# Kernel optimization log

Hardware: AMD Instinct MI355X
Metric: run time of the kernel (lower is better)

## Reference

```python
import jax, jax.numpy as jnp
import numpy as np

S, P, SAMPLE_K = 512, 512, 10          # superpoints, points per superpoint, FPS samples
NUM_MASKS, H, W = 128, 512, 512
RADIUS, MASK_THRES, SIM_THRES, N_MASK, TOP_K = 0.2, 0.2, 0.5, 5, 10
FEAT_DIM = 32


def setup_inputs() -> dict:
    key = jax.random.key(0)
    k1, k2, k3, k4, k5, k6 = jax.random.split(key, 6)
    N = S * P
    pcds = jax.random.normal(k1, (N, 3), jnp.float32) * 2.0
    spt_labels = (jnp.arange(N) // P).astype(jnp.int32)  # sorted, contiguous superpoints
    masks = jax.random.bernoulli(k2, 0.15, (NUM_MASKS, H, W))
    yx = jax.random.randint(k3, (N, 2), 0, H).astype(jnp.int32)
    vis = jax.random.randint(k4, (N, 1), 0, 2).astype(jnp.int32)
    mapping = jnp.concatenate([jnp.zeros((N, 1), jnp.int32), yx, vis], axis=1)
    sam_scores = jax.random.uniform(k5, (NUM_MASKS,), jnp.float32)
    point_feas = jax.random.normal(k6, (N, FEAT_DIM), jnp.float32)
    return {"pcds": pcds, "spt_labels": spt_labels, "masks": masks,
            "mapping": mapping, "sam_scores": sam_scores, "point_feas": point_feas}


def _fps(pts, k):
    # pts: (P,3). Deterministic first index 0 (torch uses a random first index).
    d0 = jnp.linalg.norm(pts - pts[0], axis=1)
    def step(dist, _):
        idx = jnp.argmax(dist)
        dist = jnp.minimum(dist, jnp.linalg.norm(pts - pts[idx], axis=1))
        return dist, idx
    _, idxs = jax.lax.scan(step, d0, None, length=k - 1)
    return jnp.concatenate([jnp.zeros((1,), idxs.dtype), idxs])


def reference(pcds, spt_labels, masks, mapping, sam_scores, point_feas):
    # ---- FPS representatives per superpoint (all superpoints have P>=min_points) ----
    pts_g = pcds.reshape(S, P, 3)
    idxs = jax.vmap(lambda p: _fps(p, SAMPLE_K))(pts_g)              # (S, k)
    reps = jnp.take_along_axis(pts_g, idxs[:, :, None], axis=1)      # (S, k, 3)

    # ---- pairwise min distance between superpoint rep sets -> radius adjacency ----
    flat = reps.reshape(S * SAMPLE_K, 3)
    sq = jnp.sum(flat * flat, axis=1)
    D2 = sq[:, None] + sq[None, :] - 2.0 * (flat @ flat.T)           # (S*k, S*k)
    D2 = D2.reshape(S, SAMPLE_K, S, SAMPLE_K).min(axis=(1, 3))       # (S, S)
    dmin = jnp.sqrt(jnp.maximum(D2, 1e-12))
    eye = jnp.eye(S, dtype=bool)
    adjacency = jnp.where((dmin < RADIUS) & (~eye), jnp.exp(-dmin), 0.0)

    # ---- per-point mask coverage (visible points only) ----
    y = jnp.clip(mapping[:, 1], 0, H - 1)
    x = jnp.clip(mapping[:, 2], 0, W - 1)
    vis = mapping[:, 3] == 1
    coverage = masks[:, y, x].T & vis[:, None]                       # (N, num_masks)

    # ---- aggregate coverage per superpoint, keep top_k superpoints per mask ----
    counts = coverage.reshape(S, P, NUM_MASKS).sum(axis=1)
    fraction = counts.astype(jnp.float32) / (P + 1e-6)               # (S, num_masks)
    _, top_inds = jax.lax.top_k(fraction.T, TOP_K)                   # (num_masks, top_k)
    topk_mask = jnp.zeros((NUM_MASKS, S), bool).at[
        jnp.arange(NUM_MASKS)[:, None], top_inds].set(True).T        # (S, num_masks)
    frac_kept = jnp.where(topk_mask, fraction, 0.0)
    contrib = frac_kept >= MASK_THRES                                # (S, num_masks) bool

    # ---- superpoint features (mean, L2-normalized) ----
    feats = point_feas.reshape(S, P, -1).sum(axis=1) / (P + 1e-6)
    feats = feats / jnp.maximum(jnp.linalg.norm(feats, axis=1, keepdims=True), 1e-12)

    # ---- modulate adjacency by top-n_mask mask-overlap IoU and feature similarity ----
    union = contrib[:, None, :] | contrib[None, :, :]                # (S, S, num_masks)
    _, u_inds = jax.lax.top_k(union.astype(jnp.float32), N_MASK)     # (S, S, n_mask)
    mi = jnp.take_along_axis(jnp.broadcast_to(contrib[:, None, :], union.shape), u_inds, axis=2)
    mj = jnp.take_along_axis(jnp.broadcast_to(contrib[None, :, :], union.shape), u_inds, axis=2)
    inter = (mi & mj).sum(-1).astype(jnp.float32)
    uni = (mi | mj).sum(-1).astype(jnp.float32)
    overlap = inter / (uni + 1e-6)
    sim = jnp.clip((feats @ feats.T + 1.0) / 2.0, 0.0, 1.0)
    sim = jnp.where(sim < SIM_THRES, 1.0, sim)
    mod = overlap * sim
    adjacency = jnp.where(adjacency > 0, jnp.maximum(mod, adjacency), adjacency)

    # ---- superpoint confidence scores ----
    weights = frac_kept * sam_scores[None, :]
    conf = jnp.maximum(weights.sum(1) / (frac_kept.sum(1) + 1e-6), 0.0)
    return adjacency, conf
```

## Files before the change

### kernel.cpp

```cpp
#include <hip/hip_runtime.h>
#include <cstddef>
#include <cstdint>

#define SPTS 512
#define PPS  512
#define KFPS 10
#define NMSK 128
#define HH 512
#define WW 512
#define HWPIX (HH*WW)
#define FDIM 32
#define TOPK_SEL 10
#define NMASK_TOP 5

__device__ __forceinline__ unsigned mask_val(const void* raw, long long idx, int mode) {
    if (mode == 0) return ((const unsigned char*)raw)[idx] ? 1u : 0u;
    if (mode == 1) return ((const int*)raw)[idx] ? 1u : 0u;
    return (((const float*)raw)[idx] != 0.0f) ? 1u : 0u;
}

__device__ __forceinline__ int detect_mode(const void* raw) {
    __shared__ int s_any1, s_any23;
    if (threadIdx.x == 0) { s_any1 = 0; s_any23 = 0; }
    __syncthreads();
    if (threadIdx.x < 256) {
        uint4 w = ((const uint4*)raw)[threadIdx.x];
        unsigned b1  = (w.x >> 8 | w.y >> 8 | w.z >> 8 | w.w >> 8) & 0xFFu;
        unsigned b23 = ((w.x >> 16) | (w.y >> 16) | (w.z >> 16) | (w.w >> 16)) & 0xFFFFu;
        if (b1)  atomicOr(&s_any1, 1);
        if (b23) atomicOr(&s_any23, 1);
    }
    __syncthreads();
    return s_any1 ? 0 : (s_any23 ? 2 : 1);
}

__global__ void __launch_bounds__(256) k_repack_fps(const void* raw, unsigned* maskbits,
                                                    const float* pcds, float* reps) {
    int bid = blockIdx.x;
    if (bid < 1024) {
        int mode = detect_mode(raw);
        int quarter = bid & 3;
        int ptile   = bid >> 2;
        int pix0 = ptile * 1024 + threadIdx.x * 4;
        unsigned w[4] = {0, 0, 0, 0};
        if (mode == 0) {
            const unsigned char* base = (const unsigned char*)raw + (size_t)quarter * 32 * HWPIX + pix0;
#pragma unroll
            for (int m = 0; m < 32; ++m) {
                unsigned v = *(const unsigned*)(base + (size_t)m * HWPIX);
#pragma unroll
                for (int p = 0; p < 4; ++p)
                    w[p] |= ((v >> (8 * p)) & 1u) << m;
            }
        } else {
            const unsigned* base = (const unsigned*)raw + (size_t)quarter * 32 * HWPIX + pix0;
#pragma unroll
            for (int m = 0; m < 32; ++m) {
                uint4 v = *(const uint4*)(base + (size_t)m * HWPIX);
                w[0] |= (unsigned)(v.x != 0u) << m;
                w[1] |= (unsigned)(v.y != 0u) << m;
                w[2] |= (unsigned)(v.z != 0u) << m;
                w[3] |= (unsigned)(v.w != 0u) << m;
            }
        }
#pragma unroll
        for (int p = 0; p < 4; ++p)
            maskbits[(size_t)(pix0 + p) * 4 + quarter] = w[p];
        return;
    }
    int lane = threadIdx.x & 63;
    int wv   = threadIdx.x >> 6;
    int s    = (bid - 1024) * 4 + wv;
    const float* base = pcds + (size_t)s * PPS * 3;
    float px_[8], py_[8], pz_[8];
#pragma unroll
    for (int k = 0; k < 8; ++k) {
        int p = lane + 64 * k;
        px_[k] = base[p * 3 + 0];
        py_[k] = base[p * 3 + 1];
        pz_[k] = base[p * 3 + 2];
    }
    float ax = __shfl(px_[0], 0), ay = __shfl(py_[0], 0), az = __shfl(pz_[0], 0);
    float dist[8];
#pragma unroll
    for (int k = 0; k < 8; ++k) {
        float dx = px_[k] - ax, dy = py_[k] - ay, dz = pz_[k] - az;
        dist[k] = sqrtf(dx * dx + dy * dy + dz * dz);
    }
    if (lane == 0) {
        reps[((size_t)s * KFPS + 0) * 3 + 0] = ax;
        reps[((size_t)s * KFPS + 0) * 3 + 1] = ay;
        reps[((size_t)s * KFPS + 0) * 3 + 2] = az;
    }
    for (int kk = 1; kk < KFPS; ++kk) {
        float bv = dist[0]; int bk = 0;
#pragma unroll
        for (int k = 1; k < 8; ++k)
            if (dist[k] > bv) { bv = dist[k]; bk = k; }
        float v = bv; int pidx = lane + 64 * bk;
#pragma unroll
        for (int off = 1; off < 64; off <<= 1) {
            float ov = __shfl_xor(v, off);
            int   op = __shfl_xor(pidx, off);
            if (ov > v || (ov == v && op < pidx)) { v = ov; pidx = op; }
        }
        int owner = pidx & 63, slot = pidx >> 6;
        float sx = px_[0], sy = py_[0], sz = pz_[0];
#pragma unroll
        for (int j = 1; j < 8; ++j)
            if (slot == j) { sx = px_[j]; sy = py_[j]; sz = pz_[j]; }
        sx = __shfl(sx, owner); sy = __shfl(sy, owner); sz = __shfl(sz, owner);
        if (lane == 0) {
            reps[((size_t)s * KFPS + kk) * 3 + 0] = sx;
            reps[((size_t)s * KFPS + kk) * 3 + 1] = sy;
            reps[((size_t)s * KFPS + kk) * 3 + 2] = sz;
        }
#pragma unroll
        for (int k = 0; k < 8; ++k) {
            float dx = px_[k] - sx, dy = py_[k] - sy, dz = pz_[k] - sz;
            float d = sqrtf(dx * dx + dy * dy + dz * dz);
            dist[k] = fminf(dist[k], d);
        }
    }
}

__global__ void __launch_bounds__(PPS) k_counts_feats(const int* mapping, const unsigned* maskbits,
                                                      const void* raw, int packed,
                                                      const float* feas,
                                                      int* counts, unsigned* contrib, float* feats) {
    int s = blockIdx.x;
    int t = threadIdx.x;
    if (t < 4) contrib[s * 4 + t] = 0u;
    __shared__ int cnt[NMSK];
    __shared__ float fpart[16][FDIM];
    if (t < NMSK) cnt[t] = 0;
    int mode = 0;
    if (!packed) mode = detect_mode(raw);
    __syncthreads();
    int i = s * PPS + t;
    int4 mp = ((const int4*)mapping)[i];
    int y = min(max(mp.y, 0), HH - 1);
    int x = min(max(mp.z, 0), WW - 1);
    bool vis = (mp.w == 1);
    unsigned w0 = 0, w1 = 0, w2 = 0, w3 = 0;
    if (vis) {
        if (packed) {
            uint4 v = *((const uint4*)(maskbits + (size_t)(y * WW + x) * 4));
            w0 = v.x; w1 = v.y; w2 = v.z; w3 = v.w;
        } else {
            long long pix = (long long)y * WW + x;
            for (int m = 0; m < NMSK; ++m) {
                unsigned v = mask_val(raw, (long long)m * HWPIX + pix, mode);
                if (m < 32)       w0 |= v << m;
                else if (m < 64)  w1 |= v << (m - 32);
                else if (m < 96)  w2 |= v << (m - 64);
                else              w3 |= v << (m - 96);
            }
        }
    }
    int lane = t & 63;
    unsigned ww[4] = { w0, w1, w2, w3 };
#pragma unroll
    for (int m = 0; m < NMSK; ++m) {
        unsigned bit = (ww[m >> 5] >> (m & 31)) & 1u;
        unsigned long long bal = __ballot((int)bit);
        if (lane == 0) atomicAdd(&cnt[m], (int)__popcll(bal));
    }
    {
        int g = t >> 5, d = t & 31;
        const float* fb = feas + (size_t)s * PPS * FDIM;
        float acc = 0.0f;
#pragma unroll 8
        for (int it = 0; it < 32; ++it) acc += fb[(g + 16 * it) * FDIM + d];
        fpart[g][d] = acc;
    }
    __syncthreads();
    if (t < NMSK) counts[s * NMSK + t] = cnt[t];
    if (t < FDIM) {
        float sum = 0.0f;
#pragma unroll
        for (int q = 0; q < 16; ++q) sum += fpart[q][t];
        float f = sum / 512.0f;
        float sq = f * f;
#pragma unroll
        for (int off = 16; off >= 1; off >>= 1) sq += __shfl_xor(sq, off);
        feats[s * FDIM + t] = f / fmaxf(sqrtf(sq), 1e-12f);
    }
}

__global__ void __launch_bounds__(SPTS) k_topk(const int* counts, unsigned* contrib, float* frac_kept) {
    int m = blockIdx.x;
    int s = threadIdx.x;
    __shared__ int cl[SPTS];
    cl[s] = counts[s * NMSK + m];
    __syncthreads();
    int c = cl[s];
    int rank = 0;
    for (int s2 = 0; s2 < SPTS; ++s2) {
        int c2 = cl[s2];
        rank += (c2 > c || (c2 == c && s2 < s)) ? 1 : 0;
    }
    bool sel = (rank < TOPK_SEL);
    float frac = (float)c / 512.0f;
    frac_kept[s * NMSK + m] = sel ? frac : 0.0f;
    if (sel && frac >= 0.2f)
        atomicOr(&contrib[s * 4 + (m >> 5)], 1u << (m & 31));
}

__global__ void __launch_bounds__(256) k_adjmod(const float* reps, const unsigned* contrib,
                                                const float* feats, const float* frac_kept,
                                                const float* sam, float* out) {
    if (blockIdx.x >= (SPTS * SPTS) / 256) {
        int s = (blockIdx.x - (SPTS * SPTS) / 256) * 256 + threadIdx.x;
        if (s < SPTS) {
            float sw = 0.0f, sf = 0.0f;
            for (int m = 0; m < NMSK; ++m) {
                float fk = frac_kept[s * NMSK + m];
                sw += fk * sam[m];
                sf += fk;
            }
            out[(size_t)SPTS * SPTS + s] = fmaxf(sw / (sf + 1e-6f), 0.0f);
        }
        return;
    }
    int idx = blockIdx.x * blockDim.x + threadIdx.x;
    int i = idx >> 9, j = idx & 511;
    __shared__ float ri[KFPS * 3];
    __shared__ float sqi[KFPS];
    if (threadIdx.x < KFPS * 3) ri[threadIdx.x] = reps[(size_t)i * KFPS * 3 + threadIdx.x];
    __syncthreads();
    if (threadIdx.x < KFPS) {
        float X = ri[threadIdx.x * 3], Y = ri[threadIdx.x * 3 + 1], Z = ri[threadIdx.x * 3 + 2];
        sqi[threadIdx.x] = X * X + Y * Y + Z * Z;
    }
    __syncthreads();
    float rjx[KFPS], rjy[KFPS], rjz[KFPS], sqj[KFPS];
    const float* rp = reps + (size_t)j * KFPS * 3;
#pragma unroll
    for (int b = 0; b < KFPS; ++b) {
        float X = rp[b * 3], Y = rp[b * 3 + 1], Z = rp[b * 3 + 2];
        rjx[b] = X; rjy[b] = Y; rjz[b] = Z;
        sqj[b] = X * X + Y * Y + Z * Z;
    }
    float mn = 1e30f;
#pragma unroll
    for (int a = 0; a < KFPS; ++a) {
        float ax = ri[a * 3], ay = ri[a * 3 + 1], az = ri[a * 3 + 2];
        float sa = sqi[a];
#pragma unroll
        for (int b = 0; b < KFPS; ++b) {
            float dot = ax * rjx[b] + ay * rjy[b] + az * rjz[b];
            float d2 = (sa + sqj[b]) - 2.0f * dot;
            mn = fminf(mn, d2);
        }
    }
    float dmin = sqrtf(fmaxf(mn, 1e-12f));
    float a = (dmin < 0.2f && i != j) ? expf(-dmin) : 0.0f;
    if (a > 0.0f) {
        uint4 c4i = *((const uint4*)(contrib + (size_t)i * 4));
        uint4 c4j = *((const uint4*)(contrib + (size_t)j * 4));
        unsigned cia[4] = { c4i.x, c4i.y, c4i.z, c4i.w };
        unsigned cja[4] = { c4j.x, c4j.y, c4j.z, c4j.w };
        int taken = 0, inter = 0, uni = 0;
#pragma unroll
        for (int w = 0; w < 4; ++w) {
            unsigned u = cia[w] | cja[w];
            unsigned both = cia[w] & cja[w];
            while (u && taken < NMASK_TOP) {
                unsigned bit = u & (~u + 1u);
                uni++;
                if (both & bit) inter++;
                u ^= bit; taken++;
            }
        }
        float overlap = (float)inter / ((float)uni + 1e-6f);
        const float* fi = feats + (size_t)i * FDIM;
        const float* fj = feats + (size_t)j * FDIM;
        float dot = 0.0f;
#pragma unroll
        for (int d = 0; d < FDIM; ++d) dot += fi[d] * fj[d];
        float sim = (dot + 1.0f) / 2.0f;
        sim = fminf(fmaxf(sim, 0.0f), 1.0f);
        if (sim < 0.5f) sim = 1.0f;
        a = fmaxf(overlap * sim, a);
    }
    out[idx] = a;
}

extern "C" void kernel_launch(void* const* d_in, const int* in_sizes, int n_in,
                              void* d_out, int out_size, void* d_ws, size_t ws_size,
                              hipStream_t stream) {
    const float* pcds    = (const float*)d_in[0];
    const void*  masks   = d_in[2];
    const int*   mapping = (const int*)d_in[3];
    const float* sam     = (const float*)d_in[4];
    const float* feas    = (const float*)d_in[5];
    float* out = (float*)d_out;

    char* ws = (char*)d_ws;
    size_t off = 0;
    auto take = [&](size_t bytes) -> void* {
        void* p = ws + off;
        off += (bytes + 255) & ~(size_t)255;
        return p;
    };
    float*    reps      = (float*)take((size_t)SPTS * KFPS * 3 * sizeof(float));
    int*      counts    = (int*)take((size_t)SPTS * NMSK * sizeof(int));
    unsigned* contrib   = (unsigned*)take((size_t)SPTS * 4 * sizeof(unsigned));
    float*    frac_kept = (float*)take((size_t)SPTS * NMSK * sizeof(float));
    float*    feats     = (float*)take((size_t)SPTS * FDIM * sizeof(float));
    unsigned* maskbits  = (unsigned*)take((size_t)HWPIX * 4 * sizeof(unsigned));
    size_t need_packed = off;
    int packed = (ws_size >= need_packed) ? 1 : 0;

    k_repack_fps<<<1152, 256, 0, stream>>>(masks, maskbits, pcds, reps);
    k_counts_feats<<<SPTS, PPS, 0, stream>>>(mapping, maskbits, masks, packed, feas,
                                             counts, contrib, feats);
    k_topk<<<NMSK, SPTS, 0, stream>>>(counts, contrib, frac_kept);
    k_adjmod<<<(SPTS * SPTS) / 256 + 2, 256, 0, stream>>>(reps, contrib, feats, frac_kept, sam, out);
}
```

Before: 80.50 us.

## Rebalance stages: move adjacency distance into stage2, feature means into stage1

Moves the per-superpoint feature averaging (now float4-vectorised) into the first kernel alongside mask repacking and FPS. Moves the pairwise rep-distance adjacency computation into the counts kernel so it overlaps with the bit counting, writing the base adjacency to the output. The last kernel then only reads that output and modulates the nonzero entries. Mask repacking now handles all 128 masks per thread and writes one uint4 per pixel instead of scattered 32-bit words. The cost is an extra full read of the output matrix and higher register pressure in the repack loop.

```diff
diff --git a/kernel.cpp b/kernel.cpp
--- a/kernel.cpp
+++ b/kernel.cpp
@@ -34,43 +34,7 @@
     return s_any1 ? 0 : (s_any23 ? 2 : 1);
 }
 
-__global__ void __launch_bounds__(256) k_repack_fps(const void* raw, unsigned* maskbits,
-                                                    const float* pcds, float* reps) {
-    int bid = blockIdx.x;
-    if (bid < 1024) {
-        int mode = detect_mode(raw);
-        int quarter = bid & 3;
-        int ptile   = bid >> 2;
-        int pix0 = ptile * 1024 + threadIdx.x * 4;
-        unsigned w[4] = {0, 0, 0, 0};
-        if (mode == 0) {
-            const unsigned char* base = (const unsigned char*)raw + (size_t)quarter * 32 * HWPIX + pix0;
-#pragma unroll
-            for (int m = 0; m < 32; ++m) {
-                unsigned v = *(const unsigned*)(base + (size_t)m * HWPIX);
-#pragma unroll
-                for (int p = 0; p < 4; ++p)
-                    w[p] |= ((v >> (8 * p)) & 1u) << m;
-            }
-        } else {
-            const unsigned* base = (const unsigned*)raw + (size_t)quarter * 32 * HWPIX + pix0;
-#pragma unroll
-            for (int m = 0; m < 32; ++m) {
-                uint4 v = *(const uint4*)(base + (size_t)m * HWPIX);
-                w[0] |= (unsigned)(v.x != 0u) << m;
-                w[1] |= (unsigned)(v.y != 0u) << m;
-                w[2] |= (unsigned)(v.z != 0u) << m;
-                w[3] |= (unsigned)(v.w != 0u) << m;
-            }
-        }
-#pragma unroll
-        for (int p = 0; p < 4; ++p)
-            maskbits[(size_t)(pix0 + p) * 4 + quarter] = w[p];
-        return;
-    }
-    int lane = threadIdx.x & 63;
-    int wv   = threadIdx.x >> 6;
-    int s    = (bid - 1024) * 4 + wv;
+__device__ __forceinline__ void fps_wave(const float* pcds, float* reps, int s, int lane) {
     const float* base = pcds + (size_t)s * PPS * 3;
     float px_[8], py_[8], pz_[8];
 #pragma unroll
@@ -124,67 +88,158 @@
     }
 }
 
-__global__ void __launch_bounds__(PPS) k_counts_feats(const int* mapping, const unsigned* maskbits,
-                                                      const void* raw, int packed,
-                                                      const float* feas,
-                                                      int* counts, unsigned* contrib, float* feats) {
-    int s = blockIdx.x;
+__global__ void __launch_bounds__(256) k_stage1(const void* raw, unsigned* maskbits,
+                                                const float* pcds, float* reps,
+                                                const float* feas, float* feats, int packed) {
+    int bid = blockIdx.x;
     int t = threadIdx.x;
-    if (t < 4) contrib[s * 4 + t] = 0u;
-    __shared__ int cnt[NMSK];
-    __shared__ float fpart[16][FDIM];
-    if (t < NMSK) cnt[t] = 0;
-    int mode = 0;
-    if (!packed) mode = detect_mode(raw);
-    __syncthreads();
-    int i = s * PPS + t;
-    int4 mp = ((const int4*)mapping)[i];
-    int y = min(max(mp.y, 0), HH - 1);
-    int x = min(max(mp.z, 0), WW - 1);
-    bool vis = (mp.w == 1);
-    unsigned w0 = 0, w1 = 0, w2 = 0, w3 = 0;
-    if (vis) {
-        if (packed) {
-            uint4 v = *((const uint4*)(maskbits + (size_t)(y * WW + x) * 4));
-            w0 = v.x; w1 = v.y; w2 = v.z; w3 = v.w;
+    if (bid < 256) {
+        if (!packed) return;
+        int mode = detect_mode(raw);
+        int pix0 = bid * 1024 + t * 4;
+        unsigned w[4][4] = {};
+        if (mode == 0) {
+            const unsigned char* base = (const unsigned char*)raw + pix0;
+#pragma unroll 8
+            for (int m = 0; m < NMSK; ++m) {
+                unsigned v = *(const unsigned*)(base + (size_t)m * HWPIX);
+                int q = m >> 5; unsigned sh = m & 31;
+#pragma unroll
+                for (int p = 0; p < 4; ++p)
+                    w[q][p] |= ((v >> (8 * p)) & 1u) << sh;
+            }
         } else {
-            long long pix = (long long)y * WW + x;
+            const unsigned* base = (const unsigned*)raw + pix0;
+#pragma unroll 8
             for (int m = 0; m < NMSK; ++m) {
-                unsigned v = mask_val(raw, (long long)m * HWPIX + pix, mode);
-                if (m < 32)       w0 |= v << m;
-                else if (m < 64)  w1 |= v << (m - 32);
-                else if (m < 96)  w2 |= v << (m - 64);
-                else              w3 |= v << (m - 96);
-            }
-        }
-    }
-    int lane = t & 63;
-    unsigned ww[4] = { w0, w1, w2, w3 };
-#pragma unroll
-    for (int m = 0; m < NMSK; ++m) {
-        unsigned bit = (ww[m >> 5] >> (m & 31)) & 1u;
-        unsigned long long bal = __ballot((int)bit);
-        if (lane == 0) atomicAdd(&cnt[m], (int)__popcll(bal));
+                uint4 v = *(const uint4*)(base + (size_t)m * HWPIX);
+                int q = m >> 5; unsigned sh = m & 31;
+                w[q][0] |= (unsigned)(v.x != 0u) << sh;
+                w[q][1] |= (unsigned)(v.y != 0u) << sh;
+                w[q][2] |= (unsigned)(v.z != 0u) << sh;
+                w[q][3] |= (unsigned)(v.w != 0u) << sh;
+            }
+        }
+#pragma unroll
+        for (int p = 0; p < 4; ++p) {
+            uint4 o; o.x = w[0][p]; o.y = w[1][p]; o.z = w[2][p]; o.w = w[3][p];
+            *(uint4*)(maskbits + (size_t)(pix0 + p) * 4) = o;
+        }
+        return;
+    }
+    if (bid < 384) {
+        fps_wave(pcds, reps, (bid - 256) * 4 + (t >> 6), t & 63);
+        return;
     }
     {
-        int g = t >> 5, d = t & 31;
+        int s = bid - 384;
         const float* fb = feas + (size_t)s * PPS * FDIM;
-        float acc = 0.0f;
-#pragma unroll 8
-        for (int it = 0; it < 32; ++it) acc += fb[(g + 16 * it) * FDIM + d];
-        fpart[g][d] = acc;
-    }
-    __syncthreads();
-    if (t < NMSK) counts[s * NMSK + t] = cnt[t];
-    if (t < FDIM) {
-        float sum = 0.0f;
-#pragma unroll
-        for (int q = 0; q < 16; ++q) sum += fpart[q][t];
-        float f = sum / 512.0f;
-        float sq = f * f;
-#pragma unroll
-        for (int off = 16; off >= 1; off >>= 1) sq += __shfl_xor(sq, off);
-        feats[s * FDIM + t] = f / fmaxf(sqrtf(sq), 1e-12f);
+        int c = t & 7, g = t >> 3;
+        float4 acc = { 0.0f, 0.0f, 0.0f, 0.0f };
+#pragma unroll 4
+        for (int it = 0; it < 16; ++it) {
+            int p = g + 32 * it;
+            float4 v = *(const float4*)(fb + p * FDIM + c * 4);
+            acc.x += v.x; acc.y += v.y; acc.z += v.z; acc.w += v.w;
+        }
+        __shared__ float4 fp4[32][8];
+        fp4[g][c] = acc;
+        __syncthreads();
+        if (t < FDIM) {
+            int cc = t >> 2, comp = t & 3;
+            float sum = 0.0f;
+#pragma unroll
+            for (int q = 0; q < 32; ++q) {
+                float4 v = fp4[q][cc];
+                sum += (comp == 0) ? v.x : (comp == 1) ? v.y : (comp == 2) ? v.z : v.w;
+            }
+            float f = sum / 512.0f;
+            float sq = f * f;
+#pragma unroll
+            for (int off = 16; off >= 1; off >>= 1) sq += __shfl_xor(sq, off);
+            feats[s * FDIM + t] = f / fmaxf(sqrtf(sq), 1e-12f);
+        }
+    }
+}
+
+__global__ void __launch_bounds__(512) k_stage2(const int* mapping, const unsigned* maskbits,
+                                                const void* raw, int packed, const float* reps,
+                                                int* counts, unsigned* contrib, float* out) {
+    int bid = blockIdx.x;
+    int t = threadIdx.x;
+    if (bid < SPTS) {
+        int s = bid;
+        if (t < 4) contrib[s * 4 + t] = 0u;
+        __shared__ int cnt[NMSK];
+        if (t < NMSK) cnt[t] = 0;
+        int mode = 0;
+        if (!packed) mode = detect_mode(raw);
+        __syncthreads();
+        int i = s * PPS + t;
+        int4 mp = ((const int4*)mapping)[i];
+        int y = min(max(mp.y, 0), HH - 1);
+        int x = min(max(mp.z, 0), WW - 1);
+        bool vis = (mp.w == 1);
+        unsigned w0 = 0, w1 = 0, w2 = 0, w3 = 0;
+        if (vis) {
+            if (packed) {
+                uint4 v = *((const uint4*)(maskbits + (size_t)(y * WW + x) * 4));
+                w0 = v.x; w1 = v.y; w2 = v.z; w3 = v.w;
+            } else {
+                long long pix = (long long)y * WW + x;
+                for (int m = 0; m < NMSK; ++m) {
+                    unsigned v = mask_val(raw, (long long)m * HWPIX + pix, mode);
+                    if (m < 32)       w0 |= v << m;
+                    else if (m < 64)  w1 |= v << (m - 32);
+                    else if (m < 96)  w2 |= v << (m - 64);
+                    else              w3 |= v << (m - 96);
+                }
+            }
+        }
+        int lane = t & 63;
+        unsigned ww[4] = { w0, w1, w2, w3 };
+#pragma unroll
+        for (int m = 0; m < NMSK; ++m) {
+            unsigned bit = (ww[m >> 5] >> (m & 31)) & 1u;
+            unsigned long long bal = __ballot((int)bit);
+            if (lane == 0) atomicAdd(&cnt[m], (int)__popcll(bal));
+        }
+        __syncthreads();
+        if (t < NMSK) counts[s * NMSK + t] = cnt[t];
+    } else {
+        int i = bid - SPTS;
+        __shared__ float ri[KFPS * 3];
+        __shared__ float sqi[KFPS];
+        if (t < KFPS * 3) ri[t] = reps[(size_t)i * KFPS * 3 + t];
+        __syncthreads();
+        if (t < KFPS) {
+            float X = ri[t * 3], Y = ri[t * 3 + 1], Z = ri[t * 3 + 2];
+            sqi[t] = X * X + Y * Y + Z * Z;
+        }
+        __syncthreads();
+        int j = t;
+        float rjx[KFPS], rjy[KFPS], rjz[KFPS], sqj[KFPS];
+        const float* rp = reps + (size_t)j * KFPS * 3;
+#pragma unroll
+        for (int b = 0; b < KFPS; ++b) {
+            float X = rp[b * 3], Y = rp[b * 3 + 1], Z = rp[b * 3 + 2];
+            rjx[b] = X; rjy[b] = Y; rjz[b] = Z;
+            sqj[b] = X * X + Y * Y + Z * Z;
+        }
+        float mn = 1e30f;
+#pragma unroll
+        for (int a = 0; a < KFPS; ++a) {
+            float ax = ri[a * 3], ay = ri[a * 3 + 1], az = ri[a * 3 + 2];
+            float sa = sqi[a];
+#pragma unroll
+            for (int b = 0; b < KFPS; ++b) {
+                float dot = ax * rjx[b] + ay * rjy[b] + az * rjz[b];
+                float d2 = (sa + sqj[b]) - 2.0f * dot;
+                mn = fminf(mn, d2);
+            }
+        }
+        float dmin = sqrtf(fmaxf(mn, 1e-12f));
+        out[(size_t)i * SPTS + j] = (dmin < 0.2f && i != j) ? expf(-dmin) : 0.0f;
     }
 }
 
@@ -207,9 +262,9 @@
         atomicOr(&contrib[s * 4 + (m >> 5)], 1u << (m & 31));
 }
 
-__global__ void __launch_bounds__(256) k_adjmod(const float* reps, const unsigned* contrib,
-                                                const float* feats, const float* frac_kept,
-                                                const float* sam, float* out) {
+__global__ void __launch_bounds__(256) k_modconf(const unsigned* contrib, const float* feats,
+                                                 const float* frac_kept, const float* sam,
+                                                 float* out) {
     if (blockIdx.x >= (SPTS * SPTS) / 256) {
         int s = (blockIdx.x - (SPTS * SPTS) / 256) * 256 + threadIdx.x;
         if (s < SPTS) {
@@ -225,66 +280,34 @@
     }
     int idx = blockIdx.x * blockDim.x + threadIdx.x;
     int i = idx >> 9, j = idx & 511;
-    __shared__ float ri[KFPS * 3];
-    __shared__ float sqi[KFPS];
-    if (threadIdx.x < KFPS * 3) ri[threadIdx.x] = reps[(size_t)i * KFPS * 3 + threadIdx.x];
-    __syncthreads();
-    if (threadIdx.x < KFPS) {
-        float X = ri[threadIdx.x * 3], Y = ri[threadIdx.x * 3 + 1], Z = ri[threadIdx.x * 3 + 2];
-        sqi[threadIdx.x] = X * X + Y * Y + Z * Z;
-    }
-    __syncthreads();
-    float rjx[KFPS], rjy[KFPS], rjz[KFPS], sqj[KFPS];
-    const float* rp = reps + (size_t)j * KFPS * 3;
-#pragma unroll
-    for (int b = 0; b < KFPS; ++b) {
-        float X = rp[b * 3], Y = rp[b * 3 + 1], Z = rp[b * 3 + 2];
-        rjx[b] = X; rjy[b] = Y; rjz[b] = Z;
-        sqj[b] = X * X + Y * Y + Z * Z;
-    }
-    float mn = 1e30f;
-#pragma unroll
-    for (int a = 0; a < KFPS; ++a) {
-        float ax = ri[a * 3], ay = ri[a * 3 + 1], az = ri[a * 3 + 2];
-        float sa = sqi[a];
-#pragma unroll
-        for (int b = 0; b < KFPS; ++b) {
-            float dot = ax * rjx[b] + ay * rjy[b] + az * rjz[b];
-            float d2 = (sa + sqj[b]) - 2.0f * dot;
-            mn = fminf(mn, d2);
-        }
-    }
-    float dmin = sqrtf(fmaxf(mn, 1e-12f));
-    float a = (dmin < 0.2f && i != j) ? expf(-dmin) : 0.0f;
-    if (a > 0.0f) {
-        uint4 c4i = *((const uint4*)(contrib + (size_t)i * 4));
-        uint4 c4j = *((const uint4*)(contrib + (size_t)j * 4));
-        unsigned cia[4] = { c4i.x, c4i.y, c4i.z, c4i.w };
-        unsigned cja[4] = { c4j.x, c4j.y, c4j.z, c4j.w };
-        int taken = 0, inter = 0, uni = 0;
-#pragma unroll
-        for (int w = 0; w < 4; ++w) {
-            unsigned u = cia[w] | cja[w];
-            unsigned both = cia[w] & cja[w];
-            while (u && taken < NMASK_TOP) {
-                unsigned bit = u & (~u + 1u);
-                uni++;
-                if (both & bit) inter++;
-                u ^= bit; taken++;
-            }
-        }
-        float overlap = (float)inter / ((float)uni + 1e-6f);
-        const float* fi = feats + (size_t)i * FDIM;
-        const float* fj = feats + (size_t)j * FDIM;
-        float dot = 0.0f;
-#pragma unroll
-        for (int d = 0; d < FDIM; ++d) dot += fi[d] * fj[d];
-        float sim = (dot + 1.0f) / 2.0f;
-        sim = fminf(fmaxf(sim, 0.0f), 1.0f);
-        if (sim < 0.5f) sim = 1.0f;
-        a = fmaxf(overlap * sim, a);
-    }
-    out[idx] = a;
+    float a = out[idx];
+    if (a <= 0.0f) return;
+    uint4 c4i = *((const uint4*)(contrib + (size_t)i * 4));
+    uint4 c4j = *((const uint4*)(contrib + (size_t)j * 4));
+    unsigned cia[4] = { c4i.x, c4i.y, c4i.z, c4i.w };
+    unsigned cja[4] = { c4j.x, c4j.y, c4j.z, c4j.w };
+    int taken = 0, inter = 0, uni = 0;
+#pragma unroll
+    for (int w = 0; w < 4; ++w) {
+        unsigned u = cia[w] | cja[w];
+        unsigned both = cia[w] & cja[w];
+        while (u && taken < NMASK_TOP) {
+            unsigned bit = u & (~u + 1u);
+            uni++;
+            if (both & bit) inter++;
+            u ^= bit; taken++;
+        }
+    }
+    float overlap = (float)inter / ((float)uni + 1e-6f);
+    const float* fi = feats + (size_t)i * FDIM;
+    const float* fj = feats + (size_t)j * FDIM;
+    float dot = 0.0f;
+#pragma unroll
+    for (int d = 0; d < FDIM; ++d) dot += fi[d] * fj[d];
+    float sim = (dot + 1.0f) / 2.0f;
+    sim = fminf(fmaxf(sim, 0.0f), 1.0f);
+    if (sim < 0.5f) sim = 1.0f;
+    out[idx] = fmaxf(overlap * sim, a);
 }
 
 extern "C" void kernel_launch(void* const* d_in, const int* in_sizes, int n_in,
@@ -313,9 +336,9 @@
     size_t need_packed = off;
     int packed = (ws_size >= need_packed) ? 1 : 0;
 
-    k_repack_fps<<<1152, 256, 0, stream>>>(masks, maskbits, pcds, reps);
-    k_counts_feats<<<SPTS, PPS, 0, stream>>>(mapping, maskbits, masks, packed, feas,
-                                             counts, contrib, feats);
+    k_stage1<<<896, 256, 0, stream>>>(masks, maskbits, pcds, reps, feas, feats, packed);
+    k_stage2<<<1024, 512, 0, stream>>>(mapping, maskbits, masks, packed, reps,
+                                       counts, contrib, out);
     k_topk<<<NMSK, SPTS, 0, stream>>>(counts, contrib, frac_kept);
-    k_adjmod<<<(SPTS * SPTS) / 256 + 2, 256, 0, stream>>>(reps, contrib, feats, frac_kept, sam, out);
-}
+    k_modconf<<<(SPTS * SPTS) / 256 + 2, 256, 0, stream>>>(contrib, feats, frac_kept, sam, out);
+}
```

Result: slower. 105.0 us (+30.4%).
